# Kernel optimization log

Measured on AMD Instinct MI355X. Metric: run time of the kernel, lower is better.

## Reference

```python
import jax, jax.numpy as jnp
import numpy as np
from numpy.lib.stride_tricks import sliding_window_view

# Static configuration matching init_kwargs
F_, H_, W_ = 2, 32, 32          # video_shape
K = 5                            # kernel_size (odd)
HEADS, DIM_HEAD = 8, 64
N = F_ * H_ * W_                 # number of video tokens (2048)
PAD = K // 2
INNER = HEADS * DIM_HEAD         # 512


def _neighbors():
    # Flattened token index at each (f,h,w); pad with sentinel N (out of bounds -> zeros / masked)
    idx = np.arange(N, dtype=np.int32).reshape(F_, H_, W_)
    padded = np.full((F_ + 2 * PAD, H_ + 2 * PAD, W_ + 2 * PAD), N, dtype=np.int32)
    padded[PAD:PAD + F_, PAD:PAD + H_, PAD:PAD + W_] = idx
    # sliding_window_view matches unfoldNd's kernel-offset ordering (kf, kh, kw row-major)
    return sliding_window_view(padded, (K, K, K)).reshape(N, K ** 3)


NBR = jnp.asarray(_neighbors())                                   # [N, K^3]
# causal: query i attends only to neighbors with index <= i; prepend BOS column (never masked)
CAUSAL = jnp.pad(jnp.arange(N)[:, None] < NBR, ((0, 0), (1, 0)))  # [N, K^3 + 1]


def setup_inputs() -> dict:
    key = jax.random.key(0)
    k1, k2, k3 = jax.random.split(key, 3)
    return {
        "x": jax.random.normal(k1, (1, N, INNER), jnp.float32),
        "w_qkv": jax.random.normal(k2, (INNER, 3 * INNER), jnp.float32) * 0.02,
        "w_out": jax.random.normal(k3, (INNER, INNER), jnp.float32) * 0.02,
        "b_out": jnp.zeros((INNER,), jnp.float32),
    }


def reference(x, w_qkv, w_out, b_out):
    b, n, dim = x.shape            # n == N
    bh = b * HEADS
    scale = DIM_HEAD ** -0.5

    xp = jnp.pad(x, ((0, 0), (0, 1), (0, 0)))        # pad one zero token at the end: [b, n+1, dim]
    qkv = xp @ w_qkv                                  # [b, n+1, 3*inner]
    q, kk, vv = jnp.split(qkv, 3, axis=-1)

    def split_heads(t):  # 'b n (h d) -> (b h) n d'
        return t.reshape(b, n + 1, HEADS, DIM_HEAD).transpose(0, 2, 1, 3).reshape(bh, n + 1, DIM_HEAD)

    q, kk, vv = map(split_heads, (q, kk, vv))
    q = q[:, 1:] * scale                              # drop BOS query: [bh, n, d]
    k_bos, kk = kk[:, :1], kk[:, 1:]                  # BOS kv + n spatial tokens
    v_bos, vv = vv[:, :1], vv[:, 1:]

    # Append a zero row so the sentinel index N gathers zeros (== unfold's zero padding)
    zero = jnp.zeros((bh, 1, DIM_HEAD), kk.dtype)
    kw = jnp.concatenate([kk, zero], axis=1)[:, NBR]  # [bh, n, K^3, d]
    vw = jnp.concatenate([vv, zero], axis=1)[:, NBR]

    bos_k = jnp.broadcast_to(k_bos[:, None], (bh, n, 1, DIM_HEAD))
    bos_v = jnp.broadcast_to(v_bos[:, None], (bh, n, 1, DIM_HEAD))
    kw = jnp.concatenate([bos_k, kw], axis=2)         # [bh, n, K^3+1, d]
    vw = jnp.concatenate([bos_v, vw], axis=2)

    sim = jnp.einsum('bid,bijd->bij', q, kw)          # [bh, n, K^3+1]
    sim = jnp.where(CAUSAL[:n], -jnp.finfo(sim.dtype).max, sim)
    attn = jax.nn.softmax(sim, axis=-1)
    out = jnp.einsum('bij,bijd->bid', attn, vw)       # [bh, n, d]

    out = jnp.concatenate([v_bos, out], axis=1)       # BOS output = its value: [bh, n+1, d]
    out = out.reshape(b, HEADS, n + 1, DIM_HEAD).transpose(0, 2, 1, 3).reshape(b, n + 1, INNER)
    return (out @ w_out + b_out)[:, :n]
```

## Files before the change

kernel.cpp:

```cpp
#include <hip/hip_runtime.h>
#include <hip/hip_bf16.h>

#define NTOK  2048
#define INNER 512
#define KDIM  512
#define QKVP  1536

typedef __attribute__((ext_vector_type(8))) short bf16x8;
typedef __attribute__((ext_vector_type(4))) float f32x4;

__device__ __forceinline__ unsigned short f2b(float f) {
  unsigned int u = __float_as_uint(f);
  return (unsigned short)((u + 0x7FFFu + ((u >> 16) & 1u)) >> 16);
}

__device__ __forceinline__ void async_copy16(const unsigned short* g, unsigned short* l) {
  __builtin_amdgcn_global_load_lds((const __attribute__((address_space(1))) void*)g,
                                   (__attribute__((address_space(3))) void*)l, 16, 0, 0);
}

__global__ __launch_bounds__(256) void prep(const float* __restrict__ w_qkv,
                                            const float* __restrict__ w_out,
                                            const float* __restrict__ x,
                                            unsigned short* __restrict__ wqkvT,
                                            unsigned short* __restrict__ woutT,
                                            unsigned short* __restrict__ xb,
                                            int* __restrict__ glist,
                                            int* __restrict__ gcnt) {
  __shared__ float tile[32][33];
  __shared__ int list[192];
  __shared__ int cntS;
  const int tid = threadIdx.x;
  int b = blockIdx.x;

  if (b >= 1152) {
    const int i = (b - 1152) * 1024 + tid * 4;
    float4 v = *(const float4*)(x + i);
    ushort4 o;
    o.x = f2b(v.x); o.y = f2b(v.y); o.z = f2b(v.z); o.w = f2b(v.w);
    *(ushort4*)(xb + i) = o;
    return;
  }

  if (b < 1024) {
    const float* in; unsigned short* out; int K, N, bx, by;
    if (b < 768) { in = w_qkv; out = wqkvT; K = 512; N = 1536; bx = b % 48; by = b / 48; }
    else { int bb = b - 768; in = w_out; out = woutT; K = 512; N = 512; bx = bb & 15; by = bb >> 4; }
    const int k0 = by * 32, n0 = bx * 32;
    const int r = tid >> 3, c4 = (tid & 7) * 4;
    float4 v = *(const float4*)(in + (size_t)(k0 + r) * N + n0 + c4);
    tile[r][c4 + 0] = v.x; tile[r][c4 + 1] = v.y;
    tile[r][c4 + 2] = v.z; tile[r][c4 + 3] = v.w;
    __syncthreads();
    ushort4 o;
    o.x = f2b(tile[c4 + 0][r]);
    o.y = f2b(tile[c4 + 1][r]);
    o.z = f2b(tile[c4 + 2][r]);
    o.w = f2b(tile[c4 + 3][r]);
    *(ushort4*)(out + (size_t)(n0 + r) * K + k0 + c4) = o;
    return;
  }

  const int pt = b - 1024;
  const int f  = pt >> 6;
  const int hh = (pt >> 1) & 31;
  const int w0 = (pt & 1) << 4;

  if (tid < 192) list[tid] = 0x7FFFFFFF;
  if (tid == 0) { list[0] = 0; cntS = 1; }
  __syncthreads();
  if (tid >= 1 && tid <= 160) {
    int cc = tid - 1;
    int p = cc / 20, wo = cc - p * 20;
    int ff = (p < 5) ? 0 : 1;
    int h2 = hh - 2 + ((p < 5) ? p : (p - 5));
    bool ok = (p < 5) ? ((f == 1) ? (h2 >= 0 && h2 <= 31) : (p <= 2 && h2 >= 0))
                      : (f == 1 && h2 >= 0);
    if (ok) {
      bool diag = (ff == f) && (h2 == hh);
      int wlo = max(0, w0 - 2);
      int whi = min(31, diag ? (w0 + 15) : (w0 + 17));
      int w2 = wlo + wo;
      if (w2 <= whi) {
        int pos = atomicAdd(&cntS, 1);
        list[pos] = ((ff << 10) | (h2 << 5) | w2) + 1;
      }
    }
  }
  __syncthreads();
  if (tid < 192) glist[pt * 192 + tid] = list[tid];
  if (tid == 0) gcnt[pt] = cntS;
}

__global__ __launch_bounds__(256, 4) void gemm_qkv(const unsigned short* __restrict__ A,
                                                   const unsigned short* __restrict__ Bt,
                                                   unsigned short* __restrict__ C) {
  constexpr int N = 1536, K = 512;
  __shared__ __align__(16) unsigned short As[2][64 * 32];
  __shared__ __align__(16) unsigned short Bs[2][64 * 32];
  const int tid = threadIdx.x, lane = tid & 63, wave = tid >> 6;
  const int m0 = blockIdx.y * 64, n0 = blockIdx.x * 64;
  const int wm = (wave >> 1) * 32, wn = (wave & 1) * 32;
  const int li = tid * 8, r = li >> 5, c = li & 31;
  const int fr = lane & 15, fk = (lane >> 4) * 8;

  f32x4 acc[2][2] = {};

  for (int k0 = 0; k0 < K; k0 += 64) {
    async_copy16(A  + (size_t)(m0 + r) * K + k0 + c,      &As[0][li]);
    async_copy16(A  + (size_t)(m0 + r) * K + k0 + 32 + c, &As[1][li]);
    async_copy16(Bt + (size_t)(n0 + r) * K + k0 + c,      &Bs[0][li]);
    async_copy16(Bt + (size_t)(n0 + r) * K + k0 + 32 + c, &Bs[1][li]);
    __syncthreads();
    bf16x8 af[2][2], bfr[2][2];
#pragma unroll
    for (int h = 0; h < 2; ++h) {
#pragma unroll
      for (int i = 0; i < 2; ++i) af[i][h]  = *(const bf16x8*)&As[h][(wm + i * 16 + fr) * 32 + fk];
#pragma unroll
      for (int j = 0; j < 2; ++j) bfr[j][h] = *(const bf16x8*)&Bs[h][(wn + j * 16 + fr) * 32 + fk];
    }
#pragma unroll
    for (int i = 0; i < 2; ++i)
#pragma unroll
      for (int j = 0; j < 2; ++j) {
        acc[i][j] = __builtin_amdgcn_mfma_f32_16x16x32_bf16(af[i][0], bfr[j][0], acc[i][j], 0, 0, 0);
        acc[i][j] = __builtin_amdgcn_mfma_f32_16x16x32_bf16(af[i][1], bfr[j][1], acc[i][j], 0, 0, 0);
      }
    __syncthreads();
  }

  const int er = (lane >> 4) * 4, ec = lane & 15;
#pragma unroll
  for (int i = 0; i < 2; ++i)
#pragma unroll
    for (int j = 0; j < 2; ++j) {
      const int col = n0 + wn + j * 16 + ec;
#pragma unroll
      for (int rr = 0; rr < 4; ++rr) {
        const int row = m0 + wm + i * 16 + er + rr;
        C[(size_t)row * N + col] = f2b(acc[i][j][rr]);
      }
    }
}

__global__ __launch_bounds__(256, 4) void gemm_out(const unsigned short* __restrict__ A,
                                                   const unsigned short* __restrict__ Bt,
                                                   const float* __restrict__ bias,
                                                   float* __restrict__ C) {
  constexpr int N = 512, K = 512;
  __shared__ __align__(16) unsigned short As[2][32 * 32];
  __shared__ __align__(16) unsigned short Bs[2][64 * 32];
  const int tid = threadIdx.x, lane = tid & 63, wave = tid >> 6;
  const int m0 = blockIdx.y * 32, n0 = blockIdx.x * 64;
  const int wm = (wave >> 1) * 16, wn = (wave & 1) * 32;
  const int li = tid * 8, r = li >> 5, c = li & 31;
  const int fr = lane & 15, fk = (lane >> 4) * 8;

  f32x4 acc[2] = {};

  for (int k0 = 0; k0 < K; k0 += 64) {
    if (tid < 128) {
      async_copy16(A + (size_t)(m0 + r) * K + k0 + c,      &As[0][li]);
      async_copy16(A + (size_t)(m0 + r) * K + k0 + 32 + c, &As[1][li]);
    }
    async_copy16(Bt + (size_t)(n0 + r) * K + k0 + c,      &Bs[0][li]);
    async_copy16(Bt + (size_t)(n0 + r) * K + k0 + 32 + c, &Bs[1][li]);
    __syncthreads();
    bf16x8 af[2], bfr[2][2];
#pragma unroll
    for (int h = 0; h < 2; ++h) {
      af[h] = *(const bf16x8*)&As[h][(wm + fr) * 32 + fk];
#pragma unroll
      for (int j = 0; j < 2; ++j) bfr[j][h] = *(const bf16x8*)&Bs[h][(wn + j * 16 + fr) * 32 + fk];
    }
#pragma unroll
    for (int j = 0; j < 2; ++j) {
      acc[j] = __builtin_amdgcn_mfma_f32_16x16x32_bf16(af[0], bfr[j][0], acc[j], 0, 0, 0);
      acc[j] = __builtin_amdgcn_mfma_f32_16x16x32_bf16(af[1], bfr[j][1], acc[j], 0, 0, 0);
    }
    __syncthreads();
  }

  const int er = (lane >> 4) * 4, ec = lane & 15;
#pragma unroll
  for (int j = 0; j < 2; ++j) {
    const int col = n0 + wn + j * 16 + ec;
    const float b = bias[col];
#pragma unroll
    for (int rr = 0; rr < 4; ++rr) {
      const int row = m0 + wm + er + rr;
      C[(size_t)row * N + col] = acc[j][rr] + b;
    }
  }
}

__global__ __launch_bounds__(256, 4) void attn_mfma(const unsigned short* __restrict__ qkv,
                                                    const int* __restrict__ glist,
                                                    const int* __restrict__ gcnt,
                                                    unsigned short* __restrict__ O) {
  __shared__ __align__(16) int list[192];
  __shared__ __align__(16) unsigned short Vlds[4][16 * 72];
  __shared__ __align__(16) float mOd[3][16][72];
  __shared__ float mM[3][16], mL[3][16];
  __shared__ int cntS;

  const int tid  = threadIdx.x;
  const int head = blockIdx.y;

  if (blockIdx.x == 128) {
    if (tid < 64) O[head * 64 + tid] = qkv[1024 + head * 64 + tid];
    return;
  }
  const int pt = blockIdx.x;
  const int f  = pt >> 6;
  const int hh = (pt >> 1) & 31;
  const int w0 = (pt & 1) << 4;
  const int base_i = (f << 10) | (hh << 5) | w0;

  if (tid < 192) list[tid] = glist[pt * 192 + tid];
  if (tid == 0) cntS = gcnt[pt];
  __syncthreads();
  const int nsub = (cntS + 15) >> 4;

  const int lane = tid & 63;
  const int wave = tid >> 6;
  const int quad = lane >> 4;
  const int ec   = lane & 15;

  const int i_q = base_i + ec;
  const int tq  = min(i_q + 1, 2047);
  const unsigned short* qrow = qkv + (size_t)tq * QKVP + head * 64 + quad * 8;
  const bf16x8 qb0 = *(const bf16x8*)(qrow);
  const bf16x8 qb1 = *(const bf16x8*)(qrow + 32);

  unsigned short* vbuf = &Vlds[wave][0];

  f32x4 Od[4] = {{0,0,0,0},{0,0,0,0},{0,0,0,0},{0,0,0,0}};
  float m = -1e30f, l = 0.0f;

  for (int sub = wave; sub < nsub; sub += 4) {
    const int base = sub * 16;
    const int tok_e = list[base + ec];
    const int4 tokv = *(const int4*)&list[base + quad * 4];
    const int tk[4] = {tokv.x, tokv.y, tokv.z, tokv.w};

    const int t0 = (tok_e > 2047) ? 0 : tok_e;
    const unsigned short* kr = qkv + (size_t)t0 * QKVP + 512 + head * 64 + quad * 8;
    const unsigned short* vr = qkv + (size_t)t0 * QKVP + 1024 + head * 64 + quad * 8;
    const bf16x8 kf0 = *(const bf16x8*)(kr);
    const bf16x8 kf1 = *(const bf16x8*)(kr + 32);
    const bf16x8 vs0 = *(const bf16x8*)(vr);
    const bf16x8 vs1 = *(const bf16x8*)(vr + 32);

    f32x4 S = {0, 0, 0, 0};
    S = __builtin_amdgcn_mfma_f32_16x16x32_bf16(kf0, qb0, S, 0, 0, 0);
    S = __builtin_amdgcn_mfma_f32_16x16x32_bf16(kf1, qb1, S, 0, 0, 0);

    *(bf16x8*)&vbuf[ec * 72 + quad * 8]      = vs0;
    *(bf16x8*)&vbuf[ec * 72 + 32 + quad * 8] = vs1;

    float Sm[4];
#pragma unroll
    for (int r = 0; r < 4; ++r) {
      const int tok = tk[r];
      const int idx = tok - 1;
      const bool v = (tok == 0) ||
                     ((idx <= i_q) && ((unsigned)((idx & 31) - (w0 + ec) + 2) <= 4u));
      Sm[r] = v ? S[r] * 0.125f : -1e30f;
    }
    float mx = fmaxf(fmaxf(Sm[0], Sm[1]), fmaxf(Sm[2], Sm[3]));
    mx = fmaxf(mx, __shfl_xor(mx, 16, 64));
    mx = fmaxf(mx, __shfl_xor(mx, 32, 64));
    const float mn = fmaxf(m, mx);
    const float corr = __expf(m - mn);
    m = mn;
    const float p0 = __expf(Sm[0] - mn);
    const float p1 = __expf(Sm[1] - mn);
    const float p2 = __expf(Sm[2] - mn);
    const float p3 = __expf(Sm[3] - mn);
    float rs = (p0 + p1) + (p2 + p3);
    rs += __shfl_xor(rs, 16, 64);
    rs += __shfl_xor(rs, 32, 64);
    l = l * corr + rs;

    bf16x8 pf;
    pf[0] = (short)f2b(p0); pf[1] = (short)f2b(p1);
    pf[2] = (short)f2b(p2); pf[3] = (short)f2b(p3);
    pf[4] = 0; pf[5] = 0; pf[6] = 0; pf[7] = 0;

#pragma unroll
    for (int dt = 0; dt < 4; ++dt) {
      bf16x8 vf;
#pragma unroll
      for (int j = 0; j < 4; ++j) vf[j] = (short)vbuf[(quad * 4 + j) * 72 + dt * 16 + ec];
      vf[4] = 0; vf[5] = 0; vf[6] = 0; vf[7] = 0;
#pragma unroll
      for (int r = 0; r < 4; ++r) Od[dt][r] *= corr;
      Od[dt] = __builtin_amdgcn_mfma_f32_16x16x32_bf16(vf, pf, Od[dt], 0, 0, 0);
    }
  }

  if (wave > 0) {
#pragma unroll
    for (int dt = 0; dt < 4; ++dt)
      *(f32x4*)&mOd[wave - 1][ec][dt * 16 + quad * 4] = Od[dt];
    if (quad == 0) { mM[wave - 1][ec] = m; mL[wave - 1][ec] = l; }
  }
  __syncthreads();
  if (wave == 0 && i_q <= 2046) {
    const float m1 = mM[0][ec], m2 = mM[1][ec], m3 = mM[2][ec];
    const float mm = fmaxf(fmaxf(m, m1), fmaxf(m2, m3));
    const float c0 = __expf(m - mm);
    const float c1 = __expf(m1 - mm);
    const float c2 = __expf(m2 - mm);
    const float c3 = __expf(m3 - mm);
    const float rl = 1.0f / (l * c0 + mL[0][ec] * c1 + mL[1][ec] * c2 + mL[2][ec] * c3);
    unsigned short* ob = O + (size_t)(i_q + 1) * 512 + head * 64 + quad * 4;
#pragma unroll
    for (int dt = 0; dt < 4; ++dt) {
      const f32x4 o1 = *(const f32x4*)&mOd[0][ec][dt * 16 + quad * 4];
      const f32x4 o2 = *(const f32x4*)&mOd[1][ec][dt * 16 + quad * 4];
      const f32x4 o3 = *(const f32x4*)&mOd[2][ec][dt * 16 + quad * 4];
      ushort4 u;
      u.x = f2b((Od[dt][0] * c0 + o1[0] * c1 + o2[0] * c2 + o3[0] * c3) * rl);
      u.y = f2b((Od[dt][1] * c0 + o1[1] * c1 + o2[1] * c2 + o3[1] * c3) * rl);
      u.z = f2b((Od[dt][2] * c0 + o1[2] * c1 + o2[2] * c2 + o3[2] * c3) * rl);
      u.w = f2b((Od[dt][3] * c0 + o1[3] * c1 + o2[3] * c2 + o3[3] * c3) * rl);
      *(ushort4*)(ob + dt * 16) = u;
    }
  }
}


extern "C" void kernel_launch(void* const* d_in, const int* in_sizes, int n_in,
                              void* d_out, int out_size, void* d_ws, size_t ws_size,
                              hipStream_t stream) {
  const float* x     = (const float*)d_in[0];
  const float* w_qkv = (const float*)d_in[1];
  const float* w_out = (const float*)d_in[2];
  const float* b_out = (const float*)d_in[3];
  float* out = (float*)d_out;

  char* ws = (char*)d_ws;
  unsigned short* qkvb  = (unsigned short*)(ws);
  unsigned short* wqkvT = (unsigned short*)(ws + 6291456);
  unsigned short* woutT = (unsigned short*)(ws + 7864320);
  unsigned short* Ob    = (unsigned short*)(ws + 8388608);
  unsigned short* xb    = (unsigned short*)(ws + 10485760);
  int*            glist = (int*)(ws + 12582912);
  int*            gcnt  = (int*)(ws + 12681216);

  hipLaunchKernelGGL(prep, dim3(2176), dim3(256), 0, stream,
                     w_qkv, w_out, x, wqkvT, woutT, xb, glist, gcnt);

  hipLaunchKernelGGL(gemm_qkv, dim3(24, 32), dim3(256), 0, stream, xb, wqkvT, qkvb);

  hipLaunchKernelGGL(attn_mfma, dim3(129, 8), dim3(256), 0, stream, qkvb, glist, gcnt, Ob);

  hipLaunchKernelGGL(gemm_out, dim3(8, 64), dim3(256), 0, stream, Ob, woutT, b_out, out);
}
```

Before: 89.86 us.

## Fuse x bf16 conversion into QKV GEMM and move neighbor lists into attention

```diff
diff --git a/kernel.cpp b/kernel.cpp
--- a/kernel.cpp
+++ b/kernel.cpp
@@ -3,7 +3,6 @@
 
 #define NTOK  2048
 #define INNER 512
-#define KDIM  512
 #define QKVP  1536
 
 typedef __attribute__((ext_vector_type(8))) short bf16x8;
@@ -20,35 +19,44 @@
 }
 
 __global__ __launch_bounds__(256) void prep(const float* __restrict__ w_qkv,
-                                            const float* __restrict__ w_out,
-                                            const float* __restrict__ x,
-                                            unsigned short* __restrict__ wqkvT,
-                                            unsigned short* __restrict__ woutT,
-                                            unsigned short* __restrict__ xb,
-                                            int* __restrict__ glist,
-                                            int* __restrict__ gcnt) {
+                                            unsigned short* __restrict__ wqkvT) {
   __shared__ float tile[32][33];
-  __shared__ int list[192];
-  __shared__ int cntS;
   const int tid = threadIdx.x;
-  int b = blockIdx.x;
-
-  if (b >= 1152) {
-    const int i = (b - 1152) * 1024 + tid * 4;
-    float4 v = *(const float4*)(x + i);
-    ushort4 o;
-    o.x = f2b(v.x); o.y = f2b(v.y); o.z = f2b(v.z); o.w = f2b(v.w);
-    *(ushort4*)(xb + i) = o;
-    return;
-  }
-
-  if (b < 1024) {
-    const float* in; unsigned short* out; int K, N, bx, by;
-    if (b < 768) { in = w_qkv; out = wqkvT; K = 512; N = 1536; bx = b % 48; by = b / 48; }
-    else { int bb = b - 768; in = w_out; out = woutT; K = 512; N = 512; bx = bb & 15; by = bb >> 4; }
+  const int b = blockIdx.x;
+  constexpr int K = 512, N = 1536;
+  const int bx = b % 48, by = b / 48;
+  const int k0 = by * 32, n0 = bx * 32;
+  const int r = tid >> 3, c4 = (tid & 7) * 4;
+  float4 v = *(const float4*)(w_qkv + (size_t)(k0 + r) * N + n0 + c4);
+  tile[r][c4 + 0] = v.x; tile[r][c4 + 1] = v.y;
+  tile[r][c4 + 2] = v.z; tile[r][c4 + 3] = v.w;
+  __syncthreads();
+  ushort4 o;
+  o.x = f2b(tile[c4 + 0][r]);
+  o.y = f2b(tile[c4 + 1][r]);
+  o.z = f2b(tile[c4 + 2][r]);
+  o.w = f2b(tile[c4 + 3][r]);
+  *(ushort4*)(wqkvT + (size_t)(n0 + r) * K + k0 + c4) = o;
+}
+
+__global__ __launch_bounds__(256, 4) void gemm_qkv(const float* __restrict__ X,
+                                                   const float* __restrict__ w_out,
+                                                   const unsigned short* __restrict__ Bt,
+                                                   unsigned short* __restrict__ C,
+                                                   unsigned short* __restrict__ woutT) {
+  constexpr int N = 1536, K = 512;
+  __shared__ __align__(16) unsigned short As[2][64 * 32];
+  __shared__ __align__(16) unsigned short Bs[2][64 * 32];
+  __shared__ float tile[32][33];
+  const int tid = threadIdx.x;
+  const int b = blockIdx.x;
+
+  if (b >= 768) {
+    const int bb = b - 768;
+    const int bx = bb & 15, by = bb >> 4;
     const int k0 = by * 32, n0 = bx * 32;
     const int r = tid >> 3, c4 = (tid & 7) * 4;
-    float4 v = *(const float4*)(in + (size_t)(k0 + r) * N + n0 + c4);
+    float4 v = *(const float4*)(w_out + (size_t)(k0 + r) * 512 + n0 + c4);
     tile[r][c4 + 0] = v.x; tile[r][c4 + 1] = v.y;
     tile[r][c4 + 2] = v.z; tile[r][c4 + 3] = v.w;
     __syncthreads();
@@ -57,14 +65,140 @@
     o.y = f2b(tile[c4 + 1][r]);
     o.z = f2b(tile[c4 + 2][r]);
     o.w = f2b(tile[c4 + 3][r]);
-    *(ushort4*)(out + (size_t)(n0 + r) * K + k0 + c4) = o;
+    *(ushort4*)(woutT + (size_t)(n0 + r) * 512 + k0 + c4) = o;
     return;
   }
 
-  const int pt = b - 1024;
+  const int lane = tid & 63, wave = tid >> 6;
+  const int m0 = (b / 24) * 64, n0 = (b % 24) * 64;
+  const int wm = (wave >> 1) * 32, wn = (wave & 1) * 32;
+  const int li = tid * 8;
+  const int r2 = li >> 5, c2 = li & 31;
+  const int ar = tid >> 2, ac = (tid & 3) * 8;
+  const int fr = lane & 15, fk = (lane >> 4) * 8;
+
+  const float* ax = X + (size_t)(m0 + ar) * K + ac;
+
+  f32x4 acc[2][2] = {};
+
+  for (int k0i = 0; k0i < K; k0i += 64) {
+    float4 v0 = *(const float4*)(ax + k0i);
+    float4 v1 = *(const float4*)(ax + k0i + 4);
+    float4 v2 = *(const float4*)(ax + k0i + 32);
+    float4 v3 = *(const float4*)(ax + k0i + 36);
+    async_copy16(Bt + (size_t)(n0 + r2) * K + k0i + c2,      &Bs[0][li]);
+    async_copy16(Bt + (size_t)(n0 + r2) * K + k0i + 32 + c2, &Bs[1][li]);
+    bf16x8 a0, a1;
+    a0[0] = (short)f2b(v0.x); a0[1] = (short)f2b(v0.y); a0[2] = (short)f2b(v0.z); a0[3] = (short)f2b(v0.w);
+    a0[4] = (short)f2b(v1.x); a0[5] = (short)f2b(v1.y); a0[6] = (short)f2b(v1.z); a0[7] = (short)f2b(v1.w);
+    a1[0] = (short)f2b(v2.x); a1[1] = (short)f2b(v2.y); a1[2] = (short)f2b(v2.z); a1[3] = (short)f2b(v2.w);
+    a1[4] = (short)f2b(v3.x); a1[5] = (short)f2b(v3.y); a1[6] = (short)f2b(v3.z); a1[7] = (short)f2b(v3.w);
+    *(bf16x8*)&As[0][li] = a0;
+    *(bf16x8*)&As[1][li] = a1;
+    __syncthreads();
+    bf16x8 af[2][2], bfr[2][2];
+#pragma unroll
+    for (int h = 0; h < 2; ++h) {
+#pragma unroll
+      for (int i = 0; i < 2; ++i) af[i][h]  = *(const bf16x8*)&As[h][(wm + i * 16 + fr) * 32 + fk];
+#pragma unroll
+      for (int j = 0; j < 2; ++j) bfr[j][h] = *(const bf16x8*)&Bs[h][(wn + j * 16 + fr) * 32 + fk];
+    }
+#pragma unroll
+    for (int i = 0; i < 2; ++i)
+#pragma unroll
+      for (int j = 0; j < 2; ++j) {
+        acc[i][j] = __builtin_amdgcn_mfma_f32_16x16x32_bf16(af[i][0], bfr[j][0], acc[i][j], 0, 0, 0);
+        acc[i][j] = __builtin_amdgcn_mfma_f32_16x16x32_bf16(af[i][1], bfr[j][1], acc[i][j], 0, 0, 0);
+      }
+    __syncthreads();
+  }
+
+  const int er = (lane >> 4) * 4, ec = lane & 15;
+#pragma unroll
+  for (int i = 0; i < 2; ++i)
+#pragma unroll
+    for (int j = 0; j < 2; ++j) {
+      const int col = n0 + wn + j * 16 + ec;
+#pragma unroll
+      for (int rr = 0; rr < 4; ++rr) {
+        const int row = m0 + wm + i * 16 + er + rr;
+        C[(size_t)row * N + col] = f2b(acc[i][j][rr]);
+      }
+    }
+}
+
+__global__ __launch_bounds__(256, 4) void gemm_out(const unsigned short* __restrict__ A,
+                                                   const unsigned short* __restrict__ Bt,
+                                                   const float* __restrict__ bias,
+                                                   float* __restrict__ C) {
+  constexpr int N = 512, K = 512;
+  __shared__ __align__(16) unsigned short As[2][32 * 32];
+  __shared__ __align__(16) unsigned short Bs[2][64 * 32];
+  const int tid = threadIdx.x, lane = tid & 63, wave = tid >> 6;
+  const int m0 = blockIdx.y * 32, n0 = blockIdx.x * 64;
+  const int wm = (wave >> 1) * 16, wn = (wave & 1) * 32;
+  const int li = tid * 8, r = li >> 5, c = li & 31;
+  const int fr = lane & 15, fk = (lane >> 4) * 8;
+
+  f32x4 acc[2] = {};
+
+  for (int k0 = 0; k0 < K; k0 += 64) {
+    if (tid < 128) {
+      async_copy16(A + (size_t)(m0 + r) * K + k0 + c,      &As[0][li]);
+      async_copy16(A + (size_t)(m0 + r) * K + k0 + 32 + c, &As[1][li]);
+    }
+    async_copy16(Bt + (size_t)(n0 + r) * K + k0 + c,      &Bs[0][li]);
+    async_copy16(Bt + (size_t)(n0 + r) * K + k0 + 32 + c, &Bs[1][li]);
+    __syncthreads();
+    bf16x8 af[2], bfr[2][2];
+#pragma unroll
+    for (int h = 0; h < 2; ++h) {
+      af[h] = *(const bf16x8*)&As[h][(wm + fr) * 32 + fk];
+#pragma unroll
+      for (int j = 0; j < 2; ++j) bfr[j][h] = *(const bf16x8*)&Bs[h][(wn + j * 16 + fr) * 32 + fk];
+    }
+#pragma unroll
+    for (int j = 0; j < 2; ++j) {
+      acc[j] = __builtin_amdgcn_mfma_f32_16x16x32_bf16(af[0], bfr[j][0], acc[j], 0, 0, 0);
+      acc[j] = __builtin_amdgcn_mfma_f32_16x16x32_bf16(af[1], bfr[j][1], acc[j], 0, 0, 0);
+    }
+    __syncthreads();
+  }
+
+  const int er = (lane >> 4) * 4, ec = lane & 15;
+#pragma unroll
+  for (int j = 0; j < 2; ++j) {
+    const int col = n0 + wn + j * 16 + ec;
+    const float b = bias[col];
+#pragma unroll
+    for (int rr = 0; rr < 4; ++rr) {
+      const int row = m0 + wm + er + rr;
+      C[(size_t)row * N + col] = acc[j][rr] + b;
+    }
+  }
+}
+
+__global__ __launch_bounds__(256, 4) void attn_mfma(const unsigned short* __restrict__ qkv,
+                                                    unsigned short* __restrict__ O) {
+  __shared__ __align__(16) int list[192];
+  __shared__ __align__(16) unsigned short Vlds[4][16 * 72];
+  __shared__ __align__(16) float mOd[3][16][72];
+  __shared__ float mM[3][16], mL[3][16];
+  __shared__ int cntS;
+
+  const int tid  = threadIdx.x;
+  const int head = blockIdx.y;
+
+  if (blockIdx.x == 128) {
+    if (tid < 64) O[head * 64 + tid] = qkv[1024 + head * 64 + tid];
+    return;
+  }
+  const int pt = blockIdx.x;
   const int f  = pt >> 6;
   const int hh = (pt >> 1) & 31;
   const int w0 = (pt & 1) << 4;
+  const int base_i = (f << 10) | (hh << 5) | w0;
 
   if (tid < 192) list[tid] = 0x7FFFFFFF;
   if (tid == 0) { list[0] = 0; cntS = 1; }
@@ -88,139 +222,6 @@
     }
   }
   __syncthreads();
-  if (tid < 192) glist[pt * 192 + tid] = list[tid];
-  if (tid == 0) gcnt[pt] = cntS;
-}
-
-__global__ __launch_bounds__(256, 4) void gemm_qkv(const unsigned short* __restrict__ A,
-                                                   const unsigned short* __restrict__ Bt,
-                                                   unsigned short* __restrict__ C) {
-  constexpr int N = 1536, K = 512;
-  __shared__ __align__(16) unsigned short As[2][64 * 32];
-  __shared__ __align__(16) unsigned short Bs[2][64 * 32];
-  const int tid = threadIdx.x, lane = tid & 63, wave = tid >> 6;
-  const int m0 = blockIdx.y * 64, n0 = blockIdx.x * 64;
-  const int wm = (wave >> 1) * 32, wn = (wave & 1) * 32;
-  const int li = tid * 8, r = li >> 5, c = li & 31;
-  const int fr = lane & 15, fk = (lane >> 4) * 8;
-
-  f32x4 acc[2][2] = {};
-
-  for (int k0 = 0; k0 < K; k0 += 64) {
-    async_copy16(A  + (size_t)(m0 + r) * K + k0 + c,      &As[0][li]);
-    async_copy16(A  + (size_t)(m0 + r) * K + k0 + 32 + c, &As[1][li]);
-    async_copy16(Bt + (size_t)(n0 + r) * K + k0 + c,      &Bs[0][li]);
-    async_copy16(Bt + (size_t)(n0 + r) * K + k0 + 32 + c, &Bs[1][li]);
-    __syncthreads();
-    bf16x8 af[2][2], bfr[2][2];
-#pragma unroll
-    for (int h = 0; h < 2; ++h) {
-#pragma unroll
-      for (int i = 0; i < 2; ++i) af[i][h]  = *(const bf16x8*)&As[h][(wm + i * 16 + fr) * 32 + fk];
-#pragma unroll
-      for (int j = 0; j < 2; ++j) bfr[j][h] = *(const bf16x8*)&Bs[h][(wn + j * 16 + fr) * 32 + fk];
-    }
-#pragma unroll
-    for (int i = 0; i < 2; ++i)
-#pragma unroll
-      for (int j = 0; j < 2; ++j) {
-        acc[i][j] = __builtin_amdgcn_mfma_f32_16x16x32_bf16(af[i][0], bfr[j][0], acc[i][j], 0, 0, 0);
-        acc[i][j] = __builtin_amdgcn_mfma_f32_16x16x32_bf16(af[i][1], bfr[j][1], acc[i][j], 0, 0, 0);
-      }
-    __syncthreads();
-  }
-
-  const int er = (lane >> 4) * 4, ec = lane & 15;
-#pragma unroll
-  for (int i = 0; i < 2; ++i)
-#pragma unroll
-    for (int j = 0; j < 2; ++j) {
-      const int col = n0 + wn + j * 16 + ec;
-#pragma unroll
-      for (int rr = 0; rr < 4; ++rr) {
-        const int row = m0 + wm + i * 16 + er + rr;
-        C[(size_t)row * N + col] = f2b(acc[i][j][rr]);
-      }
-    }
-}
-
-__global__ __launch_bounds__(256, 4) void gemm_out(const unsigned short* __restrict__ A,
-                                                   const unsigned short* __restrict__ Bt,
-                                                   const float* __restrict__ bias,
-                                                   float* __restrict__ C) {
-  constexpr int N = 512, K = 512;
-  __shared__ __align__(16) unsigned short As[2][32 * 32];
-  __shared__ __align__(16) unsigned short Bs[2][64 * 32];
-  const int tid = threadIdx.x, lane = tid & 63, wave = tid >> 6;
-  const int m0 = blockIdx.y * 32, n0 = blockIdx.x * 64;
-  const int wm = (wave >> 1) * 16, wn = (wave & 1) * 32;
-  const int li = tid * 8, r = li >> 5, c = li & 31;
-  const int fr = lane & 15, fk = (lane >> 4) * 8;
-
-  f32x4 acc[2] = {};
-
-  for (int k0 = 0; k0 < K; k0 += 64) {
-    if (tid < 128) {
-      async_copy16(A + (size_t)(m0 + r) * K + k0 + c,      &As[0][li]);
-      async_copy16(A + (size_t)(m0 + r) * K + k0 + 32 + c, &As[1][li]);
-    }
-    async_copy16(Bt + (size_t)(n0 + r) * K + k0 + c,      &Bs[0][li]);
-    async_copy16(Bt + (size_t)(n0 + r) * K + k0 + 32 + c, &Bs[1][li]);
-    __syncthreads();
-    bf16x8 af[2], bfr[2][2];
-#pragma unroll
-    for (int h = 0; h < 2; ++h) {
-      af[h] = *(const bf16x8*)&As[h][(wm + fr) * 32 + fk];
-#pragma unroll
-      for (int j = 0; j < 2; ++j) bfr[j][h] = *(const bf16x8*)&Bs[h][(wn + j * 16 + fr) * 32 + fk];
-    }
-#pragma unroll
-    for (int j = 0; j < 2; ++j) {
-      acc[j] = __builtin_amdgcn_mfma_f32_16x16x32_bf16(af[0], bfr[j][0], acc[j], 0, 0, 0);
-      acc[j] = __builtin_amdgcn_mfma_f32_16x16x32_bf16(af[1], bfr[j][1], acc[j], 0, 0, 0);
-    }
-    __syncthreads();
-  }
-
-  const int er = (lane >> 4) * 4, ec = lane & 15;
-#pragma unroll
-  for (int j = 0; j < 2; ++j) {
-    const int col = n0 + wn + j * 16 + ec;
-    const float b = bias[col];
-#pragma unroll
-    for (int rr = 0; rr < 4; ++rr) {
-      const int row = m0 + wm + er + rr;
-      C[(size_t)row * N + col] = acc[j][rr] + b;
-    }
-  }
-}
-
-__global__ __launch_bounds__(256, 4) void attn_mfma(const unsigned short* __restrict__ qkv,
-                                                    const int* __restrict__ glist,
-                                                    const int* __restrict__ gcnt,
-                                                    unsigned short* __restrict__ O) {
-  __shared__ __align__(16) int list[192];
-  __shared__ __align__(16) unsigned short Vlds[4][16 * 72];
-  __shared__ __align__(16) float mOd[3][16][72];
-  __shared__ float mM[3][16], mL[3][16];
-  __shared__ int cntS;
-
-  const int tid  = threadIdx.x;
-  const int head = blockIdx.y;
-
-  if (blockIdx.x == 128) {
-    if (tid < 64) O[head * 64 + tid] = qkv[1024 + head * 64 + tid];
-    return;
-  }
-  const int pt = blockIdx.x;
-  const int f  = pt >> 6;
-  const int hh = (pt >> 1) & 31;
-  const int w0 = (pt & 1) << 4;
-  const int base_i = (f << 10) | (hh << 5) | w0;
-
-  if (tid < 192) list[tid] = glist[pt * 192 + tid];
-  if (tid == 0) cntS = gcnt[pt];
-  __syncthreads();
   const int nsub = (cntS + 15) >> 4;
 
   const int lane = tid & 63;
@@ -347,16 +348,13 @@
   unsigned short* wqkvT = (unsigned short*)(ws + 6291456);
   unsigned short* woutT = (unsigned short*)(ws + 7864320);
   unsigned short* Ob    = (unsigned short*)(ws + 8388608);
-  unsigned short* xb    = (unsigned short*)(ws + 10485760);
-  int*            glist = (int*)(ws + 12582912);
-  int*            gcnt  = (int*)(ws + 12681216);
-
-  hipLaunchKernelGGL(prep, dim3(2176), dim3(256), 0, stream,
-                     w_qkv, w_out, x, wqkvT, woutT, xb, glist, gcnt);
-
-  hipLaunchKernelGGL(gemm_qkv, dim3(24, 32), dim3(256), 0, stream, xb, wqkvT, qkvb);
-
-  hipLaunchKernelGGL(attn_mfma, dim3(129, 8), dim3(256), 0, stream, qkvb, glist, gcnt, Ob);
+
+  hipLaunchKernelGGL(prep, dim3(768), dim3(256), 0, stream, w_qkv, wqkvT);
+
+  hipLaunchKernelGGL(gemm_qkv, dim3(1024), dim3(256), 0, stream,
+                     x, w_out, wqkvT, qkvb, woutT);
+
+  hipLaunchKernelGGL(attn_mfma, dim3(129, 8), dim3(256), 0, stream, qkvb, Ob);
 
   hipLaunchKernelGGL(gemm_out, dim3(8, 64), dim3(256), 0, stream, Ob, woutT, b_out, out);
 }
```

Result: no change. 91.23 us (+1.5%).

## Double-buffer LDS tiles in QKV and output GEMMs with async prefetch

Applied to the files above, without the earlier changes.

```diff
diff --git a/kernel.cpp b/kernel.cpp
--- a/kernel.cpp
+++ b/kernel.cpp
@@ -96,8 +96,8 @@
                                                    const unsigned short* __restrict__ Bt,
                                                    unsigned short* __restrict__ C) {
   constexpr int N = 1536, K = 512;
-  __shared__ __align__(16) unsigned short As[2][64 * 32];
-  __shared__ __align__(16) unsigned short Bs[2][64 * 32];
+  __shared__ __align__(16) unsigned short As[2][2][64 * 32];
+  __shared__ __align__(16) unsigned short Bs[2][2][64 * 32];
   const int tid = threadIdx.x, lane = tid & 63, wave = tid >> 6;
   const int m0 = blockIdx.y * 64, n0 = blockIdx.x * 64;
   const int wm = (wave >> 1) * 32, wn = (wave & 1) * 32;
@@ -106,19 +106,33 @@
 
   f32x4 acc[2][2] = {};
 
-  for (int k0 = 0; k0 < K; k0 += 64) {
-    async_copy16(A  + (size_t)(m0 + r) * K + k0 + c,      &As[0][li]);
-    async_copy16(A  + (size_t)(m0 + r) * K + k0 + 32 + c, &As[1][li]);
-    async_copy16(Bt + (size_t)(n0 + r) * K + k0 + c,      &Bs[0][li]);
-    async_copy16(Bt + (size_t)(n0 + r) * K + k0 + 32 + c, &Bs[1][li]);
-    __syncthreads();
+#define STG1(buf, kk)                                                              \
+  do {                                                                             \
+    async_copy16(A  + (size_t)(m0 + r) * K + (kk) + c,      &As[buf][0][li]);      \
+    async_copy16(A  + (size_t)(m0 + r) * K + (kk) + 32 + c, &As[buf][1][li]);      \
+    async_copy16(Bt + (size_t)(n0 + r) * K + (kk) + c,      &Bs[buf][0][li]);      \
+    async_copy16(Bt + (size_t)(n0 + r) * K + (kk) + 32 + c, &Bs[buf][1][li]);      \
+  } while (0)
+
+  STG1(0, 0);
+#pragma unroll
+  for (int it = 0; it < 8; ++it) {
+    const int cur = it & 1;
+    if (it < 7) {
+      STG1(cur ^ 1, (it + 1) * 64);
+      asm volatile("s_waitcnt vmcnt(4)" ::: "memory");
+    } else {
+      asm volatile("s_waitcnt vmcnt(0)" ::: "memory");
+    }
+    __builtin_amdgcn_s_barrier();
+    __builtin_amdgcn_sched_barrier(0);
     bf16x8 af[2][2], bfr[2][2];
 #pragma unroll
     for (int h = 0; h < 2; ++h) {
 #pragma unroll
-      for (int i = 0; i < 2; ++i) af[i][h]  = *(const bf16x8*)&As[h][(wm + i * 16 + fr) * 32 + fk];
-#pragma unroll
-      for (int j = 0; j < 2; ++j) bfr[j][h] = *(const bf16x8*)&Bs[h][(wn + j * 16 + fr) * 32 + fk];
+      for (int i = 0; i < 2; ++i) af[i][h]  = *(const bf16x8*)&As[cur][h][(wm + i * 16 + fr) * 32 + fk];
+#pragma unroll
+      for (int j = 0; j < 2; ++j) bfr[j][h] = *(const bf16x8*)&Bs[cur][h][(wn + j * 16 + fr) * 32 + fk];
     }
 #pragma unroll
     for (int i = 0; i < 2; ++i)
@@ -127,8 +141,9 @@
         acc[i][j] = __builtin_amdgcn_mfma_f32_16x16x32_bf16(af[i][0], bfr[j][0], acc[i][j], 0, 0, 0);
         acc[i][j] = __builtin_amdgcn_mfma_f32_16x16x32_bf16(af[i][1], bfr[j][1], acc[i][j], 0, 0, 0);
       }
-    __syncthreads();
-  }
+    __builtin_amdgcn_s_barrier();
+  }
+#undef STG1
 
   const int er = (lane >> 4) * 4, ec = lane & 15;
 #pragma unroll
@@ -149,8 +164,8 @@
                                                    const float* __restrict__ bias,
                                                    float* __restrict__ C) {
   constexpr int N = 512, K = 512;
-  __shared__ __align__(16) unsigned short As[2][32 * 32];
-  __shared__ __align__(16) unsigned short Bs[2][64 * 32];
+  __shared__ __align__(16) unsigned short As[2][2][32 * 32];
+  __shared__ __align__(16) unsigned short Bs[2][2][64 * 32];
   const int tid = threadIdx.x, lane = tid & 63, wave = tid >> 6;
   const int m0 = blockIdx.y * 32, n0 = blockIdx.x * 64;
   const int wm = (wave >> 1) * 16, wn = (wave & 1) * 32;
@@ -159,28 +174,44 @@
 
   f32x4 acc[2] = {};
 
-  for (int k0 = 0; k0 < K; k0 += 64) {
-    if (tid < 128) {
-      async_copy16(A + (size_t)(m0 + r) * K + k0 + c,      &As[0][li]);
-      async_copy16(A + (size_t)(m0 + r) * K + k0 + 32 + c, &As[1][li]);
-    }
-    async_copy16(Bt + (size_t)(n0 + r) * K + k0 + c,      &Bs[0][li]);
-    async_copy16(Bt + (size_t)(n0 + r) * K + k0 + 32 + c, &Bs[1][li]);
-    __syncthreads();
+#define STG2(buf, kk)                                                               \
+  do {                                                                              \
+    if (tid < 128) {                                                                \
+      async_copy16(A + (size_t)(m0 + r) * K + (kk) + c,      &As[buf][0][li]);      \
+      async_copy16(A + (size_t)(m0 + r) * K + (kk) + 32 + c, &As[buf][1][li]);      \
+    }                                                                               \
+    async_copy16(Bt + (size_t)(n0 + r) * K + (kk) + c,      &Bs[buf][0][li]);       \
+    async_copy16(Bt + (size_t)(n0 + r) * K + (kk) + 32 + c, &Bs[buf][1][li]);       \
+  } while (0)
+
+  STG2(0, 0);
+#pragma unroll
+  for (int it = 0; it < 8; ++it) {
+    const int cur = it & 1;
+    if (it < 7) {
+      STG2(cur ^ 1, (it + 1) * 64);
+      if (wave < 2) asm volatile("s_waitcnt vmcnt(4)" ::: "memory");
+      else          asm volatile("s_waitcnt vmcnt(2)" ::: "memory");
+    } else {
+      asm volatile("s_waitcnt vmcnt(0)" ::: "memory");
+    }
+    __builtin_amdgcn_s_barrier();
+    __builtin_amdgcn_sched_barrier(0);
     bf16x8 af[2], bfr[2][2];
 #pragma unroll
     for (int h = 0; h < 2; ++h) {
-      af[h] = *(const bf16x8*)&As[h][(wm + fr) * 32 + fk];
-#pragma unroll
-      for (int j = 0; j < 2; ++j) bfr[j][h] = *(const bf16x8*)&Bs[h][(wn + j * 16 + fr) * 32 + fk];
+      af[h] = *(const bf16x8*)&As[cur][h][(wm + fr) * 32 + fk];
+#pragma unroll
+      for (int j = 0; j < 2; ++j) bfr[j][h] = *(const bf16x8*)&Bs[cur][h][(wn + j * 16 + fr) * 32 + fk];
     }
 #pragma unroll
     for (int j = 0; j < 2; ++j) {
       acc[j] = __builtin_amdgcn_mfma_f32_16x16x32_bf16(af[0], bfr[j][0], acc[j], 0, 0, 0);
       acc[j] = __builtin_amdgcn_mfma_f32_16x16x32_bf16(af[1], bfr[j][1], acc[j], 0, 0, 0);
     }
-    __syncthreads();
-  }
+    __builtin_amdgcn_s_barrier();
+  }
+#undef STG2
 
   const int er = (lane >> 4) * 4, ec = lane & 15;
 #pragma unroll
```

Result: no change. 88.37 us (median of 2 runs) (-1.7%).
